# Kernel optimization log

Hardware: AMD Instinct MI355X
Metric: run time of the kernel (lower is better)

Reference implementation:

```python
import jax, jax.numpy as jnp
import numpy as np

B, C, H, W = 16, 256, 64, 64

def setup_inputs() -> dict:
    key = jax.random.key(0)
    ks = jax.random.split(key, 4)
    scale = 1.0 / np.sqrt(C)
    return {
        "x": jax.random.normal(ks[0], (B, C, H, W), dtype=jnp.float32),
        "w1": jax.random.normal(ks[1], (C, C), dtype=jnp.float32) * scale,
        "b1": jnp.zeros((C,), dtype=jnp.float32),
        "w2": jax.random.normal(ks[2], (C, C), dtype=jnp.float32) * scale,
        "b2": jnp.zeros((C,), dtype=jnp.float32),
        "w3": jax.random.normal(ks[3], (C, C), dtype=jnp.float32) * scale,
        "b3": jnp.zeros((C,), dtype=jnp.float32),
    }

def reference(x, w1, b1, w2, b2, w3, b3):
    b, c, h, w = x.shape
    n = h * w
    # 1x1 convs == per-pixel linear maps over channels; w has shape [C_out, C_in]
    def proj(wt, bias):
        return jnp.einsum('bchw,oc->bohw', x, wt) + bias[None, :, None, None]
    v = proj(w1, b1).reshape(b, c, n).transpose(0, 2, 1)   # [B, N, C]
    q = proj(w2, b2).reshape(b, c, n)                      # [B, C, N]
    k = proj(w3, b3).reshape(b, c, n)                      # [B, C, N]
    weight = jnp.einsum('bcn,bdn->bcd', q, k)              # [B, C, C]
    # global softmax over the entire flattened C*C matrix per batch element
    weight = jax.nn.softmax(weight.reshape(b, -1), axis=1).reshape(b, c, c)
    out = jnp.einsum('bnc,bcd->bdn', v, weight)            # [B, C, N]
    return out.reshape(x.shape)
```

## Files before the change

kernel.cpp:

```cpp
#include <hip/hip_runtime.h>


typedef unsigned short u16;
typedef __attribute__((ext_vector_type(8))) short short8;
typedef __attribute__((ext_vector_type(4))) float floatx4;

__device__ __forceinline__ u16 f2b(float f) {
  union { float f; unsigned int u; } v; v.f = f;
  unsigned int u = v.u;
  return (u16)((u + 0x7fffu + ((u >> 16) & 1u)) >> 16);
}
__device__ __forceinline__ float b2f(u16 h) {
  union { unsigned int u; float f; } v; v.u = ((unsigned int)h) << 16;
  return v.f;
}
__device__ __forceinline__ unsigned int cvt_pk_bf16(float lo, float hi) {
  unsigned int r;
  asm("v_cvt_pk_bf16_f32 %0, %1, %2" : "=v"(r) : "v"(lo), "v"(hi));
  return r;
}
__device__ __forceinline__ void gload_lds16(const u16* g, u16* l) {
  __builtin_amdgcn_global_load_lds(
      (const __attribute__((address_space(1))) unsigned int*)(const void*)g,
      (__attribute__((address_space(3))) unsigned int*)(void*)l, 16, 0, 0);
}

__global__ __launch_bounds__(256) void prep_w_kernel(
    const float* __restrict__ w1, const float* __restrict__ w2, const float* __restrict__ w3,
    u16* __restrict__ W1Th, u16* __restrict__ W2h, u16* __restrict__ W2l,
    u16* __restrict__ W3h, u16* __restrict__ W3l, float* __restrict__ xsum) {
  const int blk = blockIdx.x, t = threadIdx.x;
  if (blk == 576) {
#pragma unroll
    for (int i = 0; i < 16; ++i) xsum[t + i * 256] = 0.f;
    return;
  }
  if (blk < 64) {
    __shared__ float tile[32][33];
    const int e0 = (blk & 7) * 32, c0 = (blk >> 3) * 32;
    const int tx = t & 31, ty = t >> 5;
#pragma unroll
    for (int i = 0; i < 4; ++i)
      tile[ty + i * 8][tx] = w1[(c0 + ty + i * 8) * 256 + e0 + tx];
    __syncthreads();
#pragma unroll
    for (int i = 0; i < 4; ++i)
      W1Th[(e0 + ty + i * 8) * 256 + c0 + tx] = f2b(tile[tx][ty + i * 8]);
  } else {
    const int i = (blk - 64) * 256 + t;
    const int e = i & 0xffff;
    const float f = (i >> 16) ? w3[e] : w2[e];
    u16 h = f2b(f);
    if (i >> 16) { W3h[e] = h; W3l[e] = f2b(f - b2f(h)); }
    else         { W2h[e] = h; W2l[e] = f2b(f - b2f(h)); }
  }
}

__device__ __forceinline__ void stage8(const float4 a, const float4 b,
                                       u16* dH, u16* dL, float& xa) {
  const float f[8] = {a.x, a.y, a.z, a.w, b.x, b.y, b.z, b.w};
  union { unsigned int w[4]; uint4 q; } uh, ul;
#pragma unroll
  for (int i = 0; i < 4; ++i) {
    const unsigned int h = cvt_pk_bf16(f[2 * i], f[2 * i + 1]);
    uh.w[i] = h;
    union { unsigned int u; float ff; } h0, h1;
    h0.u = h << 16;
    h1.u = h & 0xffff0000u;
    ul.w[i] = cvt_pk_bf16(f[2 * i] - h0.ff, f[2 * i + 1] - h1.ff);
    xa += f[2 * i] + f[2 * i + 1];
  }
  *(uint4*)dH = uh.q;
  *(uint4*)dL = ul.q;
}

__global__ __launch_bounds__(512, 4) void gram_kernel(
    const float* __restrict__ x, float* __restrict__ Gp, float* __restrict__ xsum) {
  __shared__ u16 lH[2][256 * 32], lL[2][256 * 32];
  const int b = blockIdx.x >> 5, s = (blockIdx.x >> 1) & 15, mh = blockIdx.x & 1;
  const float* Xb = x + (long)b * 1048576 + s * 256;
  const int t = threadIdx.x;
  const int lane = t & 63, wave = t >> 6;
  const int quad = lane >> 4, l16 = lane & 15;
  const int wml = (wave & 1) * 64 + mh * 128;
  const int wn = (wave >> 1) * 64;
  const int r0 = t >> 2, qc = (t & 3) * 8;
  const int r1 = r0 + 128;
  const int wq = (((t & 3) ^ ((r0 >> 1) & 3))) * 8;
  const int rq = ((quad ^ ((l16 >> 1) & 3))) * 8;
  floatx4 acc[4][4] = {};
  float xa0 = 0.f, xa1 = 0.f;
  float4 p[4];
  p[0] = *(const float4*)(Xb + (long)r0 * 4096 + qc);
  p[1] = *(const float4*)(Xb + (long)r0 * 4096 + qc + 4);
  p[2] = *(const float4*)(Xb + (long)r1 * 4096 + qc);
  p[3] = *(const float4*)(Xb + (long)r1 * 4096 + qc + 4);
  stage8(p[0], p[1], lH[0] + r0 * 32 + wq, lL[0] + r0 * 32 + wq, xa0);
  stage8(p[2], p[3], lH[0] + r1 * 32 + wq, lL[0] + r1 * 32 + wq, xa1);
  __syncthreads();
  for (int kb = 0; kb < 8; ++kb) {
    const int cur = kb & 1, nxt = cur ^ 1;
    if (kb < 7) {
      const long kk = (kb + 1) * 32;
      p[0] = *(const float4*)(Xb + (long)r0 * 4096 + kk + qc);
      p[1] = *(const float4*)(Xb + (long)r0 * 4096 + kk + qc + 4);
      p[2] = *(const float4*)(Xb + (long)r1 * 4096 + kk + qc);
      p[3] = *(const float4*)(Xb + (long)r1 * 4096 + kk + qc + 4);
    }
    const u16* cH = lH[cur];
    const u16* cL = lL[cur];
    short8 ah[4], al[4];
#pragma unroll
    for (int i = 0; i < 4; ++i) {
      ah[i] = *(const short8*)(cH + (wml + i * 16 + l16) * 32 + rq);
      al[i] = *(const short8*)(cL + (wml + i * 16 + l16) * 32 + rq);
    }
#pragma unroll
    for (int j = 0; j < 4; ++j) {
      const short8 bh = *(const short8*)(cH + (wn + j * 16 + l16) * 32 + rq);
      const short8 bl = *(const short8*)(cL + (wn + j * 16 + l16) * 32 + rq);
#pragma unroll
      for (int i = 0; i < 4; ++i) {
        acc[i][j] = __builtin_amdgcn_mfma_f32_16x16x32_bf16(ah[i], bh, acc[i][j], 0, 0, 0);
        acc[i][j] = __builtin_amdgcn_mfma_f32_16x16x32_bf16(ah[i], bl, acc[i][j], 0, 0, 0);
        acc[i][j] = __builtin_amdgcn_mfma_f32_16x16x32_bf16(al[i], bh, acc[i][j], 0, 0, 0);
      }
    }
    if (kb < 7) {
      stage8(p[0], p[1], lH[nxt] + r0 * 32 + wq, lL[nxt] + r0 * 32 + wq, xa0);
      stage8(p[2], p[3], lH[nxt] + r1 * 32 + wq, lL[nxt] + r1 * 32 + wq, xa1);
    }
    __syncthreads();
  }
  if (mh == 0) {
    float v = xa0;
    v += __shfl_xor(v, 1);
    v += __shfl_xor(v, 2);
    if ((t & 3) == 0) atomicAdd(&xsum[b * 256 + r0], v);
    v = xa1;
    v += __shfl_xor(v, 1);
    v += __shfl_xor(v, 2);
    if ((t & 3) == 0) atomicAdd(&xsum[b * 256 + r1], v);
  }
  float* G = Gp + ((long)b * 16 + s) * 65536;
#pragma unroll
  for (int i = 0; i < 4; ++i) {
    const int row0 = wml + i * 16 + quad * 4;
#pragma unroll
    for (int j = 0; j < 4; ++j) {
      const int col = wn + j * 16 + l16;
#pragma unroll
      for (int r = 0; r < 4; ++r)
        G[(long)(row0 + r) * 256 + col] = acc[i][j][r];
    }
  }
}

__global__ __launch_bounds__(256) void reduce_g_kernel(
    const float* __restrict__ Gp, u16* __restrict__ Gh, u16* __restrict__ Gl) {
  const long e = ((long)blockIdx.x * 256 + threadIdx.x) * 4;
  const long base = ((e >> 16) << 20) + (e & 65535);
  float4 s = {0.f, 0.f, 0.f, 0.f};
#pragma unroll
  for (int i = 0; i < 16; ++i) {
    const float4 v = *(const float4*)(Gp + base + (long)i * 65536);
    s.x += v.x; s.y += v.y; s.z += v.z; s.w += v.w;
  }
  union { u16 h[4]; uint2 q; } oh, ol;
  const float sv[4] = {s.x, s.y, s.z, s.w};
#pragma unroll
  for (int c = 0; c < 4; ++c) {
    const u16 h = f2b(sv[c]);
    oh.h[c] = h;
    ol.h[c] = f2b(sv[c] - b2f(h));
  }
  *(uint2*)(Gh + e) = oh.q;
  *(uint2*)(Gl + e) = ol.q;
}

template <bool X3, int EPI>
__global__ __launch_bounds__(256) void gemm_small(
    const u16* __restrict__ Ah, const u16* __restrict__ Al,
    const u16* __restrict__ Bh, const u16* __restrict__ Bl,
    long aBatch, long bBatch, long oBatch,
    float* __restrict__ outF, u16* __restrict__ outH, u16* __restrict__ outL) {
  constexpr int LW = 264;
  __shared__ u16 smem[(X3 ? 4 : 2) * 64 * LW];
  u16* lAh = smem;
  u16* lBh = smem + 64 * LW;
  u16* lAl = X3 ? (smem + 2 * 64 * LW) : nullptr;
  u16* lBl = X3 ? (smem + 3 * 64 * LW) : nullptr;
  const int b = blockIdx.z;
  const int tm = blockIdx.x & 3, tn = blockIdx.x >> 2;
  const u16* Ahb = Ah + (long)b * aBatch + (long)tm * 64 * 256;
  const u16* Bhb = Bh + (long)b * bBatch + (long)tn * 64 * 256;
  const int t = threadIdx.x;
  const int lane = t & 63, wave = t >> 6;
  const int quad = lane >> 4, l16 = lane & 15;
  const int wm = (wave & 1) * 32, wn = (wave >> 1) * 32;
  const int r = t >> 2, c4 = t & 3;
  {
    uint4 tmp[8];
#pragma unroll
    for (int j = 0; j < 8; ++j)
      tmp[j] = *(const uint4*)(Ahb + (long)r * 256 + (c4 + 4 * j) * 8);
#pragma unroll
    for (int j = 0; j < 8; ++j)
      *(uint4*)(lAh + r * LW + (c4 + 4 * j) * 8) = tmp[j];
#pragma unroll
    for (int j = 0; j < 8; ++j)
      tmp[j] = *(const uint4*)(Bhb + (long)r * 256 + (c4 + 4 * j) * 8);
#pragma unroll
    for (int j = 0; j < 8; ++j)
      *(uint4*)(lBh + r * LW + (c4 + 4 * j) * 8) = tmp[j];
    if (X3) {
      const u16* Alb = Al + (long)b * aBatch + (long)tm * 64 * 256;
      const u16* Blb = Bl + (long)b * bBatch + (long)tn * 64 * 256;
#pragma unroll
      for (int j = 0; j < 8; ++j)
        tmp[j] = *(const uint4*)(Alb + (long)r * 256 + (c4 + 4 * j) * 8);
#pragma unroll
      for (int j = 0; j < 8; ++j)
        *(uint4*)(lAl + r * LW + (c4 + 4 * j) * 8) = tmp[j];
#pragma unroll
      for (int j = 0; j < 8; ++j)
        tmp[j] = *(const uint4*)(Blb + (long)r * 256 + (c4 + 4 * j) * 8);
#pragma unroll
      for (int j = 0; j < 8; ++j)
        *(uint4*)(lBl + r * LW + (c4 + 4 * j) * 8) = tmp[j];
    }
  }
  __syncthreads();
  floatx4 acc[2][2] = {};
#pragma unroll
  for (int kk = 0; kk < 8; ++kk) {
    const int co = kk * 32 + quad * 8;
    short8 afh[2], bfh[2];
#pragma unroll
    for (int i = 0; i < 2; ++i) {
      afh[i] = *(const short8*)(lAh + (wm + i * 16 + l16) * LW + co);
      bfh[i] = *(const short8*)(lBh + (wn + i * 16 + l16) * LW + co);
    }
    if (X3) {
      short8 afl[2], bfl[2];
#pragma unroll
      for (int i = 0; i < 2; ++i) {
        afl[i] = *(const short8*)(lAl + (wm + i * 16 + l16) * LW + co);
        bfl[i] = *(const short8*)(lBl + (wn + i * 16 + l16) * LW + co);
      }
#pragma unroll
      for (int i = 0; i < 2; ++i)
#pragma unroll
        for (int j = 0; j < 2; ++j) {
          acc[i][j] = __builtin_amdgcn_mfma_f32_16x16x32_bf16(afh[i], bfh[j], acc[i][j], 0, 0, 0);
          acc[i][j] = __builtin_amdgcn_mfma_f32_16x16x32_bf16(afh[i], bfl[j], acc[i][j], 0, 0, 0);
          acc[i][j] = __builtin_amdgcn_mfma_f32_16x16x32_bf16(afl[i], bfh[j], acc[i][j], 0, 0, 0);
        }
    } else {
#pragma unroll
      for (int i = 0; i < 2; ++i)
#pragma unroll
        for (int j = 0; j < 2; ++j)
          acc[i][j] = __builtin_amdgcn_mfma_f32_16x16x32_bf16(afh[i], bfh[j], acc[i][j], 0, 0, 0);
    }
  }
  const long obase = (long)b * oBatch;
#pragma unroll
  for (int i = 0; i < 2; ++i) {
    const int mb = tm * 64 + wm + i * 16 + quad * 4;
#pragma unroll
    for (int j = 0; j < 2; ++j) {
      const int n = tn * 64 + wn + j * 16 + l16;
#pragma unroll
      for (int rr = 0; rr < 4; ++rr) {
        const float v = acc[i][j][rr];
        const long idx = obase + (long)(mb + rr) * 256 + n;
        if (EPI == 0) {
          outF[idx] = v;
        } else if (EPI == 1) {
          u16 h = f2b(v);
          outH[idx] = h;
          outL[idx] = f2b(v - b2f(h));
        } else {
          outH[idx] = f2b(v);
        }
      }
    }
  }
}

__global__ __launch_bounds__(512, 2) void gemm_out(
    const u16* __restrict__ Mh, const float* __restrict__ x,
    const float* __restrict__ bb, float* __restrict__ out) {
  __shared__ u16 lA[2][256 * 32];
  __shared__ u16 lB[128 * 40];
  const int b = blockIdx.z;
  const int tn = blockIdx.x;
  const u16* Ab = Mh + (long)b * 65536;
  const float* Xb = x + (long)b * 1048576 + tn * 128;
  const int t = threadIdx.x;
  const int lane = t & 63, wave = t >> 6;
  const int quad = lane >> 4, l16 = lane & 15;
  const int wm = (wave & 3) * 64;
  const int wn = (wave >> 2) * 64;
  const int erp = (t >> 5) * 2;
  const int n0 = t & 31;
  const int ra = t >> 2;
  const int sc = ((t & 3) ^ ((t >> 3) & 3)) * 8;
  const int rqA = (quad ^ ((l16 >> 1) & 3)) * 8;
  u16* wA0 = &lA[0][0] + wave * 16 * 32;
  u16* wA1 = &lA[1][0] + wave * 16 * 32;
  floatx4 acc[4][4] = {};
  float pb[8];
  gload_lds16(Ab + (long)ra * 256 + sc, wA0);
  gload_lds16(Ab + (long)(ra + 128) * 256 + sc, wA0 + 128 * 32);
#pragma unroll
  for (int i = 0; i < 4; ++i) {
    pb[i]     = Xb[(long)erp * 4096 + n0 + 32 * i];
    pb[4 + i] = Xb[(long)(erp + 1) * 4096 + n0 + 32 * i];
  }
  for (int s = 0; s < 8; ++s) {
    const int kk = s * 32;
    const u16* curA = lA[s & 1];
    __syncthreads();
#pragma unroll
    for (int i = 0; i < 4; ++i) {
      const int nl = n0 + 32 * i;
      const int sb = (erp >> 3) ^ ((nl >> 4) & 3);
      *(unsigned int*)(lB + nl * 40 + sb * 8 + (erp & 7)) =
          cvt_pk_bf16(pb[i], pb[4 + i]);
    }
    __syncthreads();
    if (s < 7) {
      const int k2 = kk + 32;
      u16* nA = (s & 1) ? wA0 : wA1;
      gload_lds16(Ab + (long)ra * 256 + k2 + sc, nA);
      gload_lds16(Ab + (long)(ra + 128) * 256 + k2 + sc, nA + 128 * 32);
#pragma unroll
      for (int i = 0; i < 4; ++i) {
        pb[i]     = Xb[(long)(k2 + erp) * 4096 + n0 + 32 * i];
        pb[4 + i] = Xb[(long)(k2 + erp + 1) * 4096 + n0 + 32 * i];
      }
    }
    short8 af[4];
#pragma unroll
    for (int i = 0; i < 4; ++i)
      af[i] = *(const short8*)(curA + (wm + i * 16 + l16) * 32 + rqA);
#pragma unroll
    for (int j = 0; j < 4; ++j) {
      const int n = wn + j * 16 + l16;
      const int rb = quad ^ ((n >> 4) & 3);
      const short8 bf = *(const short8*)(lB + n * 40 + rb * 8);
#pragma unroll
      for (int i = 0; i < 4; ++i)
        acc[i][j] = __builtin_amdgcn_mfma_f32_16x16x32_bf16(af[i], bf, acc[i][j], 0, 0, 0);
    }
  }
  const long obase = (long)b * 1048576;
#pragma unroll
  for (int i = 0; i < 4; ++i) {
    const int mb = wm + i * 16 + quad * 4;
#pragma unroll
    for (int j = 0; j < 4; ++j) {
      const int n = tn * 128 + wn + j * 16 + l16;
#pragma unroll
      for (int r = 0; r < 4; ++r)
        out[obase + (long)(mb + r) * 4096 + n] = acc[i][j][r] + bb[b * 256 + mb + r];
    }
  }
}

__global__ __launch_bounds__(512) void bias_prep_kernel(
    const float* __restrict__ w2, const float* __restrict__ w3,
    const float* __restrict__ xsum, float* __restrict__ S2, float* __restrict__ S3) {
  __shared__ float xs[256];
  const int b = blockIdx.x, t = threadIdx.x;
  if (t < 256) xs[t] = xsum[b * 256 + t];
  __syncthreads();
  const float* wm = (t < 256) ? w2 : w3;
  const int a = t & 255;
  float s = 0.f;
#pragma unroll 4
  for (int c = 0; c < 256; ++c) s += wm[a * 256 + c] * xs[c];
  if (t < 256) S2[b * 256 + a] = s;
  else         S3[b * 256 + a] = s;
}

__global__ __launch_bounds__(256) void softmax_pass1(
    const float* __restrict__ Lt, const float* __restrict__ S2, const float* __restrict__ S3,
    const float* __restrict__ b2, const float* __restrict__ b3,
    float* __restrict__ bm, float* __restrict__ bs) {
  __shared__ float ls2[256], lb2[256];
  __shared__ float redm[4], reds[4];
  const int b = blockIdx.y, blk = blockIdx.x, t = threadIdx.x;
  ls2[t] = S2[b * 256 + t];
  lb2[t] = b2[t];
  __syncthreads();
  const int fw0 = blk * 2048 + t * 8;
  const int d = fw0 >> 8, a0 = fw0 & 255;
  const float c1 = b3[d];
  const float c0 = S3[b * 256 + d] + 4096.f * c1;
  const long base = (long)b * 65536 + fw0;
  float4 v0 = *(const float4*)(Lt + base);
  float4 v1 = *(const float4*)(Lt + base + 4);
  float v[8] = {v0.x, v0.y, v0.z, v0.w, v1.x, v1.y, v1.z, v1.w};
  float m = -3.4e38f;
#pragma unroll
  for (int i = 0; i < 8; ++i) {
    v[i] += lb2[a0 + i] * c0 + c1 * ls2[a0 + i];
    m = fmaxf(m, v[i]);
  }
  for (int o = 32; o; o >>= 1) m = fmaxf(m, __shfl_xor(m, o));
  const int wid = t >> 6, lane = t & 63;
  if (lane == 0) redm[wid] = m;
  __syncthreads();
  const float bmax = fmaxf(fmaxf(redm[0], redm[1]), fmaxf(redm[2], redm[3]));
  float s = 0.f;
#pragma unroll
  for (int i = 0; i < 8; ++i) s += __expf(v[i] - bmax);
  for (int o = 32; o; o >>= 1) s += __shfl_xor(s, o);
  if (lane == 0) reds[wid] = s;
  __syncthreads();
  if (t == 0) {
    bm[b * 32 + blk] = bmax;
    bs[b * 32 + blk] = reds[0] + reds[1] + reds[2] + reds[3];
  }
}

__global__ __launch_bounds__(256) void softmax_pass3(
    const float* __restrict__ Lt, const float* __restrict__ S2, const float* __restrict__ S3,
    const float* __restrict__ b2, const float* __restrict__ b3,
    const float* __restrict__ bm, const float* __restrict__ bs,
    const float* __restrict__ b1, u16* __restrict__ WTh, float* __restrict__ bb) {
  __shared__ float ls2[256], lb2[256], lb1[256];
  __shared__ float sM, sInv;
  const int b = blockIdx.y, blk = blockIdx.x, t = threadIdx.x;
  if (t < 64) {
    const float m = (t < 32) ? bm[b * 32 + t] : -3.4e38f;
    float s = (t < 32) ? bs[b * 32 + t] : 0.f;
    float M = m;
    for (int o = 32; o; o >>= 1) M = fmaxf(M, __shfl_xor(M, o));
    s *= __expf(m - M);
    for (int o = 32; o; o >>= 1) s += __shfl_xor(s, o);
    if (t == 0) { sM = M; sInv = 1.0f / s; }
  }
  ls2[t] = S2[b * 256 + t];
  lb2[t] = b2[t];
  lb1[t] = b1[t];
  __syncthreads();
  const float M = sM, inv = sInv;
  const int fw0 = blk * 2048 + t * 8;
  const int d = fw0 >> 8, a0 = fw0 & 255;
  const float c1 = b3[d];
  const float c0 = S3[b * 256 + d] + 4096.f * c1;
  const long base = (long)b * 65536 + fw0;
  float4 v0 = *(const float4*)(Lt + base);
  float4 v1 = *(const float4*)(Lt + base + 4);
  float v[8] = {v0.x, v0.y, v0.z, v0.w, v1.x, v1.y, v1.z, v1.w};
  union { u16 h[8]; uint4 q; } o;
  float bsum = 0.f;
#pragma unroll
  for (int i = 0; i < 8; ++i) {
    const float vv = v[i] + lb2[a0 + i] * c0 + c1 * ls2[a0 + i];
    const float w = __expf(vv - M) * inv;
    o.h[i] = f2b(w);
    bsum += w * lb1[a0 + i];
  }
  *(uint4*)(WTh + base) = o.q;
  for (int off = 16; off; off >>= 1) bsum += __shfl_xor(bsum, off);
  if ((t & 31) == 0) bb[b * 256 + d] = bsum;
}

extern "C" void kernel_launch(void* const* d_in, const int* in_sizes, int n_in,
                              void* d_out, int out_size, void* d_ws, size_t ws_size,
                              hipStream_t stream) {
  const float* x  = (const float*)d_in[0];
  const float* w1 = (const float*)d_in[1];
  const float* b1 = (const float*)d_in[2];
  const float* w2 = (const float*)d_in[3];
  const float* b2 = (const float*)d_in[4];
  const float* w3 = (const float*)d_in[5];
  const float* b3 = (const float*)d_in[6];
  float* out = (float*)d_out;

  char* ws = (char*)d_ws;
  size_t off = 0;
  auto alloc = [&](size_t bytes) {
    void* p = ws + off;
    off += (bytes + 255) & ~(size_t)255;
    return p;
  };
  float* Gp = (float*)alloc(16ull * 16 * 65536 * 4);
  float* xsum = (float*)alloc(16 * 256 * 4);
  u16* Gh   = (u16*)alloc(16ull * 65536 * 2);
  u16* Gl   = (u16*)alloc(16ull * 65536 * 2);
  u16* T3h  = (u16*)alloc(16ull * 65536 * 2);
  u16* T3l  = (u16*)alloc(16ull * 65536 * 2);
  float* Lb = (float*)alloc(16ull * 65536 * 4);
  u16* WTh  = (u16*)alloc(16ull * 65536 * 2);
  u16* Mh   = (u16*)alloc(16ull * 65536 * 2);
  u16* W1Th = (u16*)alloc(65536 * 2);
  u16* W2h  = (u16*)alloc(65536 * 2);
  u16* W2l  = (u16*)alloc(65536 * 2);
  u16* W3h  = (u16*)alloc(65536 * 2);
  u16* W3l  = (u16*)alloc(65536 * 2);
  float* S2   = (float*)alloc(16 * 256 * 4);
  float* S3   = (float*)alloc(16 * 256 * 4);
  float* bmx  = (float*)alloc(16 * 32 * 4);
  float* bsx  = (float*)alloc(16 * 32 * 4);
  float* bb   = (float*)alloc(16 * 256 * 4);

  prep_w_kernel<<<577, 256, 0, stream>>>(w1, w2, w3, W1Th, W2h, W2l, W3h, W3l, xsum);

  gram_kernel<<<512, 512, 0, stream>>>(x, Gp, xsum);
  reduce_g_kernel<<<1024, 256, 0, stream>>>(Gp, Gh, Gl);

  gemm_small<true, 1><<<dim3(16, 1, 16), 256, 0, stream>>>(
      W3h, W3l, Gh, Gl, 0, 65536, 65536, nullptr, T3h, T3l);
  gemm_small<true, 0><<<dim3(16, 1, 16), 256, 0, stream>>>(
      T3h, T3l, W2h, W2l, 65536, 0, 65536, Lb, nullptr, nullptr);

  bias_prep_kernel<<<16, 512, 0, stream>>>(w2, w3, xsum, S2, S3);
  softmax_pass1<<<dim3(32, 16), 256, 0, stream>>>(Lb, S2, S3, b2, b3, bmx, bsx);
  softmax_pass3<<<dim3(32, 16), 256, 0, stream>>>(Lb, S2, S3, b2, b3, bmx, bsx,
                                                  b1, WTh, bb);

  gemm_small<false, 2><<<dim3(16, 1, 16), 256, 0, stream>>>(
      WTh, nullptr, W1Th, nullptr, 65536, 0, 65536, nullptr, Mh, nullptr);
  gemm_out<<<dim3(32, 1, 16), 512, 0, stream>>>(Mh, x, bb, out);
}
```

Baseline: 217.1 us.

## Fuse softmax partial max/sum into logits GEMM epilogue; stagger gram k-order

The first softmax pass is folded into the epilogue of the second small GEMM. Each 64x64 tile adds the bias terms, reduces its block max and exp-sum, and writes 16 partials per batch instead of 32, so the separate pass that re-read the logits from memory is removed. bias_prep moves earlier so S2/S3 are ready before that GEMM runs. Separately, the gram kernel rotates its k-chunk start by slice index, which may spread concurrent blocks' loads across memory channels. The epilogue now uses scattered scalar loads of bias vectors and two extra block syncs.

```diff
diff --git a/kernel.cpp b/kernel.cpp
--- a/kernel.cpp
+++ b/kernel.cpp
@@ -88,20 +88,24 @@
   const int r1 = r0 + 128;
   const int wq = (((t & 3) ^ ((r0 >> 1) & 3))) * 8;
   const int rq = ((quad ^ ((l16 >> 1) & 3))) * 8;
+  const int ph = s & 7;
   floatx4 acc[4][4] = {};
   float xa0 = 0.f, xa1 = 0.f;
   float4 p[4];
-  p[0] = *(const float4*)(Xb + (long)r0 * 4096 + qc);
-  p[1] = *(const float4*)(Xb + (long)r0 * 4096 + qc + 4);
-  p[2] = *(const float4*)(Xb + (long)r1 * 4096 + qc);
-  p[3] = *(const float4*)(Xb + (long)r1 * 4096 + qc + 4);
+  {
+    const long k0 = ph * 32;
+    p[0] = *(const float4*)(Xb + (long)r0 * 4096 + k0 + qc);
+    p[1] = *(const float4*)(Xb + (long)r0 * 4096 + k0 + qc + 4);
+    p[2] = *(const float4*)(Xb + (long)r1 * 4096 + k0 + qc);
+    p[3] = *(const float4*)(Xb + (long)r1 * 4096 + k0 + qc + 4);
+  }
   stage8(p[0], p[1], lH[0] + r0 * 32 + wq, lL[0] + r0 * 32 + wq, xa0);
   stage8(p[2], p[3], lH[0] + r1 * 32 + wq, lL[0] + r1 * 32 + wq, xa1);
   __syncthreads();
   for (int kb = 0; kb < 8; ++kb) {
     const int cur = kb & 1, nxt = cur ^ 1;
     if (kb < 7) {
-      const long kk = (kb + 1) * 32;
+      const long kk = (long)(((kb + 1 + ph) & 7) * 32);
       p[0] = *(const float4*)(Xb + (long)r0 * 4096 + kk + qc);
       p[1] = *(const float4*)(Xb + (long)r0 * 4096 + kk + qc + 4);
       p[2] = *(const float4*)(Xb + (long)r1 * 4096 + kk + qc);
@@ -183,9 +187,13 @@
     const u16* __restrict__ Ah, const u16* __restrict__ Al,
     const u16* __restrict__ Bh, const u16* __restrict__ Bl,
     long aBatch, long bBatch, long oBatch,
-    float* __restrict__ outF, u16* __restrict__ outH, u16* __restrict__ outL) {
+    float* __restrict__ outF, u16* __restrict__ outH, u16* __restrict__ outL,
+    const float* __restrict__ S2, const float* __restrict__ S3,
+    const float* __restrict__ b2v, const float* __restrict__ b3v,
+    float* __restrict__ bm, float* __restrict__ bs) {
   constexpr int LW = 264;
   __shared__ u16 smem[(X3 ? 4 : 2) * 64 * LW];
+  __shared__ float rm[4], rs[4];
   u16* lAh = smem;
   u16* lBh = smem + 64 * LW;
   u16* lAl = X3 ? (smem + 2 * 64 * LW) : nullptr;
@@ -265,6 +273,48 @@
     }
   }
   const long obase = (long)b * oBatch;
+  if (EPI == 3) {
+    float vals[2][2][4];
+    float vmax = -3.4e38f;
+#pragma unroll
+    for (int i = 0; i < 2; ++i) {
+      const int mb = tm * 64 + wm + i * 16 + quad * 4;
+#pragma unroll
+      for (int rr = 0; rr < 4; ++rr) {
+        const int d = mb + rr;
+        const float c1 = b3v[d];
+        const float c0 = S3[b * 256 + d] + 4096.f * c1;
+#pragma unroll
+        for (int j = 0; j < 2; ++j) {
+          const int a = tn * 64 + wn + j * 16 + l16;
+          const float raw = acc[i][j][rr];
+          const float vv = raw + b2v[a] * c0 + c1 * S2[b * 256 + a];
+          vals[i][j][rr] = vv;
+          vmax = fmaxf(vmax, vv);
+          outF[obase + (long)d * 256 + a] = raw;
+        }
+      }
+    }
+    for (int o = 32; o; o >>= 1) vmax = fmaxf(vmax, __shfl_xor(vmax, o));
+    if (lane == 0) rm[wave] = vmax;
+    __syncthreads();
+    const float bmax = fmaxf(fmaxf(rm[0], rm[1]), fmaxf(rm[2], rm[3]));
+    float se = 0.f;
+#pragma unroll
+    for (int i = 0; i < 2; ++i)
+#pragma unroll
+      for (int j = 0; j < 2; ++j)
+#pragma unroll
+        for (int rr = 0; rr < 4; ++rr) se += __expf(vals[i][j][rr] - bmax);
+    for (int o = 32; o; o >>= 1) se += __shfl_xor(se, o);
+    if (lane == 0) rs[wave] = se;
+    __syncthreads();
+    if (t == 0) {
+      bm[b * 16 + blockIdx.x] = bmax;
+      bs[b * 16 + blockIdx.x] = rs[0] + rs[1] + rs[2] + rs[3];
+    }
+    return;
+  }
 #pragma unroll
   for (int i = 0; i < 2; ++i) {
     const int mb = tm * 64 + wm + i * 16 + quad * 4;
@@ -386,47 +436,6 @@
   else         S3[b * 256 + a] = s;
 }
 
-__global__ __launch_bounds__(256) void softmax_pass1(
-    const float* __restrict__ Lt, const float* __restrict__ S2, const float* __restrict__ S3,
-    const float* __restrict__ b2, const float* __restrict__ b3,
-    float* __restrict__ bm, float* __restrict__ bs) {
-  __shared__ float ls2[256], lb2[256];
-  __shared__ float redm[4], reds[4];
-  const int b = blockIdx.y, blk = blockIdx.x, t = threadIdx.x;
-  ls2[t] = S2[b * 256 + t];
-  lb2[t] = b2[t];
-  __syncthreads();
-  const int fw0 = blk * 2048 + t * 8;
-  const int d = fw0 >> 8, a0 = fw0 & 255;
-  const float c1 = b3[d];
-  const float c0 = S3[b * 256 + d] + 4096.f * c1;
-  const long base = (long)b * 65536 + fw0;
-  float4 v0 = *(const float4*)(Lt + base);
-  float4 v1 = *(const float4*)(Lt + base + 4);
-  float v[8] = {v0.x, v0.y, v0.z, v0.w, v1.x, v1.y, v1.z, v1.w};
-  float m = -3.4e38f;
-#pragma unroll
-  for (int i = 0; i < 8; ++i) {
-    v[i] += lb2[a0 + i] * c0 + c1 * ls2[a0 + i];
-    m = fmaxf(m, v[i]);
-  }
-  for (int o = 32; o; o >>= 1) m = fmaxf(m, __shfl_xor(m, o));
-  const int wid = t >> 6, lane = t & 63;
-  if (lane == 0) redm[wid] = m;
-  __syncthreads();
-  const float bmax = fmaxf(fmaxf(redm[0], redm[1]), fmaxf(redm[2], redm[3]));
-  float s = 0.f;
-#pragma unroll
-  for (int i = 0; i < 8; ++i) s += __expf(v[i] - bmax);
-  for (int o = 32; o; o >>= 1) s += __shfl_xor(s, o);
-  if (lane == 0) reds[wid] = s;
-  __syncthreads();
-  if (t == 0) {
-    bm[b * 32 + blk] = bmax;
-    bs[b * 32 + blk] = reds[0] + reds[1] + reds[2] + reds[3];
-  }
-}
-
 __global__ __launch_bounds__(256) void softmax_pass3(
     const float* __restrict__ Lt, const float* __restrict__ S2, const float* __restrict__ S3,
     const float* __restrict__ b2, const float* __restrict__ b3,
@@ -436,8 +445,8 @@
   __shared__ float sM, sInv;
   const int b = blockIdx.y, blk = blockIdx.x, t = threadIdx.x;
   if (t < 64) {
-    const float m = (t < 32) ? bm[b * 32 + t] : -3.4e38f;
-    float s = (t < 32) ? bs[b * 32 + t] : 0.f;
+    const float m = (t < 16) ? bm[b * 16 + t] : -3.4e38f;
+    float s = (t < 16) ? bs[b * 16 + t] : 0.f;
     float M = m;
     for (int o = 32; o; o >>= 1) M = fmaxf(M, __shfl_xor(M, o));
     s *= __expf(m - M);
@@ -506,8 +515,8 @@
   u16* W3l  = (u16*)alloc(65536 * 2);
   float* S2   = (float*)alloc(16 * 256 * 4);
   float* S3   = (float*)alloc(16 * 256 * 4);
-  float* bmx  = (float*)alloc(16 * 32 * 4);
-  float* bsx  = (float*)alloc(16 * 32 * 4);
+  float* bmx  = (float*)alloc(16 * 16 * 4);
+  float* bsx  = (float*)alloc(16 * 16 * 4);
   float* bb   = (float*)alloc(16 * 256 * 4);
 
   prep_w_kernel<<<577, 256, 0, stream>>>(w1, w2, w3, W1Th, W2h, W2l, W3h, W3l, xsum);
@@ -515,17 +524,20 @@
   gram_kernel<<<512, 512, 0, stream>>>(x, Gp, xsum);
   reduce_g_kernel<<<1024, 256, 0, stream>>>(Gp, Gh, Gl);
 
+  bias_prep_kernel<<<16, 512, 0, stream>>>(w2, w3, xsum, S2, S3);
+
   gemm_small<true, 1><<<dim3(16, 1, 16), 256, 0, stream>>>(
-      W3h, W3l, Gh, Gl, 0, 65536, 65536, nullptr, T3h, T3l);
-  gemm_small<true, 0><<<dim3(16, 1, 16), 256, 0, stream>>>(
-      T3h, T3l, W2h, W2l, 65536, 0, 65536, Lb, nullptr, nullptr);
-
-  bias_prep_kernel<<<16, 512, 0, stream>>>(w2, w3, xsum, S2, S3);
-  softmax_pass1<<<dim3(32, 16), 256, 0, stream>>>(Lb, S2, S3, b2, b3, bmx, bsx);
+      W3h, W3l, Gh, Gl, 0, 65536, 65536, nullptr, T3h, T3l,
+      nullptr, nullptr, nullptr, nullptr, nullptr, nullptr);
+  gemm_small<true, 3><<<dim3(16, 1, 16), 256, 0, stream>>>(
+      T3h, T3l, W2h, W2l, 65536, 0, 65536, Lb, nullptr, nullptr,
+      S2, S3, b2, b3, bmx, bsx);
+
   softmax_pass3<<<dim3(32, 16), 256, 0, stream>>>(Lb, S2, S3, b2, b3, bmx, bsx,
                                                   b1, WTh, bb);
 
   gemm_small<false, 2><<<dim3(16, 1, 16), 256, 0, stream>>>(
-      WTh, nullptr, W1Th, nullptr, 65536, 0, 65536, nullptr, Mh, nullptr);
+      WTh, nullptr, W1Th, nullptr, 65536, 0, 65536, nullptr, Mh, nullptr,
+      nullptr, nullptr, nullptr, nullptr, nullptr, nullptr);
   gemm_out<<<dim3(32, 1, 16), 512, 0, stream>>>(Mh, x, bb, out);
 }
```

Result: no change. 213.2 us (-1.8%).
